# Performance work log

Hardware: AMD Instinct MI355X
Metric: run time of the kernel (lower is better)

## Reference

```python
import jax, jax.numpy as jnp
import numpy as np

B, HGT, WID, D, NS = 4, 64, 128, 128, 2
LN_EPS = 1e-5

def layer_norm(x, g, b):
    m = jnp.mean(x, axis=-1, keepdims=True)
    v = jnp.mean((x - m) ** 2, axis=-1, keepdims=True)
    return (x - m) * jax.lax.rsqrt(v + LN_EPS) * g + b

def setup_inputs() -> dict:
    key = jax.random.key(0)
    ks = jax.random.split(key, 8)
    src = jax.random.normal(ks[0], (B, HGT * WID, D), jnp.float32)
    L = (HGT // NS) * (WID // NS)  # 2048
    s = 0.05
    return {
        "source": src,
        "target": src,  # identical -> self-attention branch in original
        "shifted_window_attn_mask": jax.random.normal(ks[1], (NS * NS, L, L), jnp.float32),
        "shifted_window_attn_mask_1d": jnp.zeros((NS, WID // NS, WID // NS), jnp.float32),
        "height": HGT,
        "width": WID,
        "attn_num_splits": NS,
        "with_shift": 1,
        "Wq": jax.random.normal(ks[2], (D, D), jnp.float32) * s,
        "Wk": jax.random.normal(ks[3], (D, D), jnp.float32) * s,
        "Wv": jax.random.normal(ks[4], (D, D), jnp.float32) * s,
        "Wm": jax.random.normal(ks[5], (D, D), jnp.float32) * s,
        "g1": jnp.ones((D,), jnp.float32),
        "b1": jnp.zeros((D,), jnp.float32),
        "W1": jax.random.normal(ks[6], (2 * D, 8 * D), jnp.float32) * s,
        "W2": jax.random.normal(ks[7], (8 * D, D), jnp.float32) * s,
        "g2": jnp.ones((D,), jnp.float32),
        "b2": jnp.zeros((D,), jnp.float32),
    }

def _shifted_window_self_attn(q, k, v, ns, with_shift, h, w, attn_mask):
    b, _, c = q.shape
    hh, ww = h // ns, w // ns  # window sizes
    sh, sw = hh // 2, ww // 2
    L = hh * ww

    def to_windows(x):
        x = x.reshape(b, h, w, c)
        if with_shift:
            x = jnp.roll(x, shift=(-sh, -sw), axis=(1, 2))
        # (b, ns, hh, ns, ww, c) -> (b*ns*ns, hh*ww, c)
        x = x.reshape(b, ns, hh, ns, ww, c).transpose(0, 1, 3, 2, 4, 5)
        return x.reshape(b * ns * ns, L, c)

    qw, kw, vw = to_windows(q), to_windows(k), to_windows(v)
    scores = jnp.einsum("bqc,bkc->bqk", qw, kw) / (c ** 0.5)  # (b*ns^2, L, L)
    if with_shift:
        scores = (scores.reshape(b, ns * ns, L, L) + attn_mask).reshape(b * ns * ns, L, L)
    attn = jax.nn.softmax(scores, axis=-1)
    out = jnp.einsum("bqk,bkc->bqc", attn, vw)
    # merge windows back
    out = out.reshape(b, ns, ns, hh, ww, c).transpose(0, 1, 3, 2, 4, 5).reshape(b, h, w, c)
    if with_shift:
        out = jnp.roll(out, shift=(sh, sw), axis=(1, 2))
    return out.reshape(b, h * w, c)

def reference(source, target, shifted_window_attn_mask, shifted_window_attn_mask_1d,
              height, width, attn_num_splits, with_shift,
              Wq, Wk, Wv, Wm, g1, b1, W1, W2, g2, b2):
    # target == source -> self-attention, attn_num_splits > 1 -> shifted-window path
    q = source @ Wq
    k = target @ Wk
    v = target @ Wv
    message = _shifted_window_self_attn(q, k, v, attn_num_splits, with_shift,
                                        height, width, shifted_window_attn_mask)
    message = layer_norm(message @ Wm, g1, b1)
    h = jnp.concatenate([source, message], axis=-1)  # (B, HW, 2D)
    message = jax.nn.gelu(h @ W1, approximate=False) @ W2
    message = layer_norm(message, g2, b2)
    return source + message
```

## Files before the change

kernel.cpp:

```cpp
#include <hip/hip_runtime.h>

typedef unsigned short u16;
typedef __bf16 bf16x8 __attribute__((ext_vector_type(8)));
typedef float f32x4 __attribute__((ext_vector_type(4)));

#define MFMA(a, b, c) __builtin_amdgcn_mfma_f32_16x16x32_bf16(a, b, c, 0, 0, 0)


__device__ __forceinline__ u16 f2b(float f) {
  unsigned u = __builtin_bit_cast(unsigned, f);
  u += 0x7fffu + ((u >> 16) & 1u);
  return (u16)(u >> 16);
}
__device__ __forceinline__ float b2f(u16 h) {
  unsigned u = (unsigned)h << 16;
  return __builtin_bit_cast(float, u);
}
__device__ __forceinline__ void glds16(const u16* g, u16* l) {
  __builtin_amdgcn_global_load_lds((const __attribute__((address_space(1))) void*)g,
                                   (__attribute__((address_space(3))) void*)l, 16, 0, 0);
}

#define QW_OFF   ((size_t)0)
#define KW_OFF   ((size_t)8 << 20)
#define VBUF_OFF ((size_t)16 << 20)
#define O1_OFF   ((size_t)24 << 20)
#define O2_OFF   ((size_t)40 << 20)
#define HID_OFF  ((size_t)0)
#define SRCB_OFF ((size_t)64 << 20)
#define MSG1_OFF ((size_t)72 << 20)
#define L1_OFF   ((size_t)80 << 20)
#define L2P_OFF  (((size_t)80 << 20) + 131072)
#define WQT_OFF  (((size_t)80 << 20) + 262144)
#define WKT_OFF  (WQT_OFF + 32768)
#define WVT_OFF  (WQT_OFF + 65536)
#define WMT_OFF  (WQT_OFF + 98304)
#define W1T_OFF  (WQT_OFF + 131072)
#define W2T_OFF  (WQT_OFF + 655360)

__global__ void k_prep(const float* __restrict__ wq, const float* __restrict__ wk,
                       const float* __restrict__ wv, const float* __restrict__ wm,
                       const float* __restrict__ w1, const float* __restrict__ w2,
                       u16* __restrict__ wqt, u16* __restrict__ wkt,
                       u16* __restrict__ wvt, u16* __restrict__ wmt,
                       u16* __restrict__ w1t, u16* __restrict__ w2t) {
  int t = blockIdx.x * 256 + threadIdx.x;
  if (t < 65536) {
    int m = t >> 14, loc = t & 16383;
    int n = loc >> 7, k = loc & 127;
    const float* s = (m == 0) ? wq : (m == 1) ? wk : (m == 2) ? wv : wm;
    u16* d = (m == 0) ? wqt : (m == 1) ? wkt : (m == 2) ? wvt : wmt;
    const float sc = (m == 0) ? 0.08838834764831845f : 1.0f;
    d[n * 128 + k] = f2b(s[k * 128 + n] * sc);
  } else if (t < 65536 + 262144) {
    int loc = t - 65536;
    int n = loc >> 8, k = loc & 255;
    w1t[n * 256 + k] = f2b(w1[k * 1024 + n]);
  } else if (t < 65536 + 262144 + 131072) {
    int loc = t - 327680;
    int n = loc >> 10, k = loc & 1023;
    w2t[n * 1024 + k] = f2b(w2[k * 128 + n]);
  }
}

__global__ __launch_bounds__(256, 2)
void k_qkv(const float* __restrict__ src,
           const u16* __restrict__ wtq, const u16* __restrict__ wtk,
           const u16* __restrict__ wtv,
           u16* __restrict__ qw, u16* __restrict__ kw, u16* __restrict__ vbuf,
           u16* __restrict__ srcb) {
  __shared__ __align__(16) u16 At[64 * 136];
  __shared__ __align__(16) u16 Bt[128 * 136];
  const int tid = threadIdx.x, bid = blockIdx.x;
  const int lane = tid & 63, wid = tid >> 6;
  const int l15 = lane & 15, quad = lane >> 4;

  {
    const int row = tid >> 2, part = tid & 3;
    const int t = bid * 64 + row;
    const int g = t >> 11, p = t & 2047;
    const int b = g >> 2, wi = (g >> 1) & 1, wj = g & 1;
    const int ii = p >> 6, jj = p & 63;
    const int y = (wi * 32 + ii + 16) & 63;
    const int x = (wj * 64 + jj + 32) & 127;
    const int srow = b * 8192 + y * 128 + x;
    const float4* sp = (const float4*)(src + srow * 128) + part * 8;
    u16* lp = &At[row * 136 + part * 32];
    u16* gp = srcb + srow * 128 + part * 32;
#pragma unroll
    for (int q = 0; q < 8; ++q) {
      float4 v = sp[q];
      ushort4 h = make_ushort4(f2b(v.x), f2b(v.y), f2b(v.z), f2b(v.w));
      *(ushort4*)(lp + q * 4) = h;
      *(ushort4*)(gp + q * 4) = h;
    }
  }
  __syncthreads();

  bf16x8 afrag[4];
  const int arow = wid * 16 + l15;
#pragma unroll
  for (int kk = 0; kk < 4; ++kk)
    afrag[kk] = *(const bf16x8*)&At[arow * 136 + kk * 32 + quad * 8];

  const f32x4 fz = {0.f, 0.f, 0.f, 0.f};
#pragma unroll 1
  for (int m = 0; m < 3; ++m) {
    const u16* wp = (m == 0) ? wtq : (m == 1) ? wtk : wtv;
    {
      const int n = tid >> 1, half = tid & 1;
      const uint4* sp = (const uint4*)(wp + n * 128 + half * 64);
      uint4* dp = (uint4*)&Bt[n * 136 + half * 64];
#pragma unroll
      for (int q = 0; q < 8; ++q) dp[q] = sp[q];
    }
    __syncthreads();
    f32x4 acc[8];
#pragma unroll
    for (int nt = 0; nt < 8; ++nt) acc[nt] = fz;
#pragma unroll
    for (int kk = 0; kk < 4; ++kk) {
#pragma unroll
      for (int nt = 0; nt < 8; ++nt) {
        bf16x8 bfr = *(const bf16x8*)&Bt[(nt * 16 + l15) * 136 + kk * 32 + quad * 8];
        acc[nt] = MFMA(afrag[kk], bfr, acc[nt]);
      }
    }
    const int t0 = bid * 64 + wid * 16 + quad * 4;
    if (m < 2) {
      u16* dst = (m == 0) ? qw : kw;
#pragma unroll
      for (int nt = 0; nt < 8; ++nt) {
        const int d = nt * 16 + l15;
#pragma unroll
        for (int r = 0; r < 4; ++r) dst[(t0 + r) * 128 + d] = f2b(acc[nt][r]);
      }
    } else {
      const int g = bid >> 5;
      const int p0 = t0 & 2047;
#pragma unroll
      for (int nt = 0; nt < 8; ++nt) {
        const int d = nt * 16 + l15;
        ushort4 hv = make_ushort4(f2b(acc[nt][0]), f2b(acc[nt][1]),
                                  f2b(acc[nt][2]), f2b(acc[nt][3]));
        *(ushort4*)&vbuf[g * 262144 + d * 2048 + p0] = hv;
      }
    }
    __syncthreads();
  }
}

__global__ __launch_bounds__(256, 2)
void k_attn(const u16* __restrict__ qw, const u16* __restrict__ kw,
            const u16* __restrict__ vbuf, const float* __restrict__ mask,
            u16* __restrict__ o1, u16* __restrict__ o2,
            float* __restrict__ l1, float* __restrict__ l2) {
  __shared__ __align__(16) u16 Kt[2][64 * 128];
  __shared__ __align__(16) u16 Vt[2][128 * 64];
  __shared__ __align__(16) u16 Pt[128 * 40];
  const int tid = threadIdx.x;
  const int bid = (blockIdx.x & 7) * 64 + (blockIdx.x >> 3);
  const int lane = tid & 63, wid = tid >> 6;
  const int l15 = lane & 15, quad = lane >> 4;
  const int b = bid & 3, w = (bid >> 2) & 3, half = (bid >> 4) & 1, qb = bid >> 5;
  const int g = b * 4 + w;
  const int k0 = half * 1024;
  const u16* kbase = kw + g * 262144 + k0 * 128;
  const u16* vbase = vbuf + g * 262144 + k0;
  const int qrow0 = qb * 128 + wid * 32;
  const float* mlane = mask + (size_t)w * 4194304 + (size_t)(qrow0 + quad * 4) * 2048 + k0 + l15;

  int offk[4], offv[4], dstb[4];
#pragma unroll
  for (int j = 0; j < 4; ++j) {
    const int s = wid * 256 + j * 64 + lane;
    const int rk = s >> 4, bk = (s & 15) ^ (rk & 15);
    offk[j] = rk * 128 + bk * 8;
    const int dv = s >> 3, bv = (s & 7) ^ (dv & 7);
    offv[j] = dv * 2048 + bv * 8;
    dstb[j] = (wid * 256 + j * 64) * 8;
  }

  bf16x8 qfrag[2][4];
#pragma unroll
  for (int qs = 0; qs < 2; ++qs) {
    const u16* qp = qw + g * 262144 + (qrow0 + qs * 16 + l15) * 128 + quad * 8;
#pragma unroll
    for (int kk = 0; kk < 4; ++kk) qfrag[qs][kk] = *(const bf16x8*)(qp + kk * 32);
  }
  const f32x4 fz = {0.f, 0.f, 0.f, 0.f};
  f32x4 o[2][8];
#pragma unroll
  for (int qs = 0; qs < 2; ++qs)
#pragma unroll
    for (int nt = 0; nt < 8; ++nt) o[qs][nt] = fz;
  float lr[2][4] = {{0.f, 0.f, 0.f, 0.f}, {0.f, 0.f, 0.f, 0.f}};
  const float L2E = 1.4426950408889634f;

#pragma unroll
  for (int j = 0; j < 4; ++j) {
    glds16(kbase + offk[j], &Kt[0][dstb[j]]);
    glds16(vbase + offv[j], &Vt[0][dstb[j]]);
  }
  float mpf[16];
#pragma unroll
  for (int qs = 0; qs < 2; ++qs)
#pragma unroll
    for (int ntl = 0; ntl < 2; ++ntl)
#pragma unroll
      for (int r = 0; r < 4; ++r)
        mpf[qs * 8 + ntl * 4 + r] = mlane[(qs * 16 + r) * 2048 + ntl * 16];

#pragma unroll 1
  for (int kt = 0; kt < 16; ++kt) {
    const int p = kt & 1;
    __syncthreads();
    if (kt < 15) {
      const u16* kb = kbase + (kt + 1) * 8192;
      const u16* vb = vbase + (kt + 1) * 64;
#pragma unroll
      for (int j = 0; j < 4; ++j) {
        glds16(kb + offk[j], &Kt[p ^ 1][dstb[j]]);
        glds16(vb + offv[j], &Vt[p ^ 1][dstb[j]]);
      }
    }
#pragma unroll
    for (int ks = 0; ks < 2; ++ks) {
      float mn[16];
      const bool hasn = (kt < 15) || (ks == 0);
      const int ncol = kt * 64 + 32 + ks * 32;
      if (hasn) {
#pragma unroll
        for (int qs = 0; qs < 2; ++qs)
#pragma unroll
          for (int ntl = 0; ntl < 2; ++ntl)
#pragma unroll
            for (int r = 0; r < 4; ++r)
              mn[qs * 8 + ntl * 4 + r] = mlane[(qs * 16 + r) * 2048 + ncol + ntl * 16];
      }
      f32x4 s[2][2];
#pragma unroll
      for (int qs = 0; qs < 2; ++qs)
#pragma unroll
        for (int ntl = 0; ntl < 2; ++ntl)
#pragma unroll
          for (int r = 0; r < 4; ++r) s[qs][ntl][r] = mpf[qs * 8 + ntl * 4 + r];
#pragma unroll
      for (int kk = 0; kk < 4; ++kk)
#pragma unroll
        for (int ntl = 0; ntl < 2; ++ntl) {
          bf16x8 kfr = *(const bf16x8*)&Kt[p][(ks * 32 + ntl * 16 + l15) * 128 +
                                             (((kk * 4 + quad) ^ l15) * 8)];
          s[0][ntl] = MFMA(qfrag[0][kk], kfr, s[0][ntl]);
          s[1][ntl] = MFMA(qfrag[1][kk], kfr, s[1][ntl]);
        }
#pragma unroll
      for (int qs = 0; qs < 2; ++qs)
#pragma unroll
        for (int ntl = 0; ntl < 2; ++ntl)
#pragma unroll
          for (int r = 0; r < 4; ++r) {
            const float pv = exp2f(s[qs][ntl][r] * L2E);
            lr[qs][r] += pv;
            Pt[(wid * 32 + qs * 16 + quad * 4 + r) * 40 + ntl * 16 + l15] = f2b(pv);
          }
      bf16x8 pf0 = *(const bf16x8*)&Pt[(wid * 32 + l15) * 40 + quad * 8];
      bf16x8 pf1 = *(const bf16x8*)&Pt[(wid * 32 + 16 + l15) * 40 + quad * 8];
#pragma unroll
      for (int nt = 0; nt < 8; ++nt) {
        bf16x8 vfr = *(const bf16x8*)&Vt[p][(nt * 16 + l15) * 64 +
                                            (((ks * 4 + quad) ^ (l15 & 7)) * 8)];
        o[0][nt] = MFMA(pf0, vfr, o[0][nt]);
        o[1][nt] = MFMA(pf1, vfr, o[1][nt]);
      }
      if (hasn) {
#pragma unroll
        for (int i = 0; i < 16; ++i) mpf[i] = mn[i];
      }
    }
  }

#pragma unroll
  for (int off = 1; off < 16; off <<= 1)
#pragma unroll
    for (int qs = 0; qs < 2; ++qs)
#pragma unroll
      for (int r = 0; r < 4; ++r) lr[qs][r] += __shfl_xor(lr[qs][r], off, 16);
  u16* op = half ? o2 : o1;
  float* lp = half ? l2 : l1;
#pragma unroll
  for (int qs = 0; qs < 2; ++qs) {
    const int t0 = g * 2048 + qrow0 + qs * 16 + quad * 4;
#pragma unroll
    for (int r = 0; r < 4; ++r) {
      const float inv = 1.f / lr[qs][r];
#pragma unroll
      for (int nt = 0; nt < 8; ++nt)
        op[(size_t)(t0 + r) * 128 + nt * 16 + l15] = f2b(o[qs][nt][r] * inv);
      if (l15 == 0) lp[t0 + r] = lr[qs][r];
    }
  }
}

__global__ __launch_bounds__(256, 2)
void k_wmln(const u16* __restrict__ o1, const u16* __restrict__ o2,
            const float* __restrict__ l1, const float* __restrict__ l2,
            const u16* __restrict__ wmt, const float* __restrict__ g1,
            const float* __restrict__ b1, u16* __restrict__ msg1) {
  __shared__ __align__(16) u16 At[64 * 136];
  __shared__ __align__(16) u16 Bt[128 * 136];
  const int tid = threadIdx.x, bid = blockIdx.x;
  const int lane = tid & 63, wid = tid >> 6;
  const int l15 = lane & 15, quad = lane >> 4;
  {
    const int row = tid >> 2, part = tid & 3;
    const int m = bid * 64 + row;
    const float la = l1[m], lb = l2[m];
    const float wA = la / (la + lb), wB = lb / (la + lb);
    const u16* p1 = o1 + (size_t)m * 128 + part * 32;
    const u16* p2 = o2 + (size_t)m * 128 + part * 32;
    u16* lp = &At[row * 136 + part * 32];
#pragma unroll
    for (int q = 0; q < 4; ++q) {
      ushort4 xa = *(const ushort4*)(p1 + q * 8);
      ushort4 xb = *(const ushort4*)(p1 + q * 8 + 4);
      ushort4 ya = *(const ushort4*)(p2 + q * 8);
      ushort4 yb = *(const ushort4*)(p2 + q * 8 + 4);
      ushort4 ha = make_ushort4(f2b(b2f(xa.x) * wA + b2f(ya.x) * wB),
                                f2b(b2f(xa.y) * wA + b2f(ya.y) * wB),
                                f2b(b2f(xa.z) * wA + b2f(ya.z) * wB),
                                f2b(b2f(xa.w) * wA + b2f(ya.w) * wB));
      ushort4 hb = make_ushort4(f2b(b2f(xb.x) * wA + b2f(yb.x) * wB),
                                f2b(b2f(xb.y) * wA + b2f(yb.y) * wB),
                                f2b(b2f(xb.z) * wA + b2f(yb.z) * wB),
                                f2b(b2f(xb.w) * wA + b2f(yb.w) * wB));
      *(ushort4*)(lp + q * 8) = ha;
      *(ushort4*)(lp + q * 8 + 4) = hb;
    }
  }
  {
    const int n = tid >> 1, half = tid & 1;
    const uint4* sp = (const uint4*)(wmt + n * 128 + half * 64);
    uint4* dp = (uint4*)&Bt[n * 136 + half * 64];
#pragma unroll
    for (int q = 0; q < 8; ++q) dp[q] = sp[q];
  }
  __syncthreads();
  bf16x8 afrag[4];
  const int arow = wid * 16 + l15;
#pragma unroll
  for (int kk = 0; kk < 4; ++kk)
    afrag[kk] = *(const bf16x8*)&At[arow * 136 + kk * 32 + quad * 8];
  const f32x4 fz = {0.f, 0.f, 0.f, 0.f};
  f32x4 acc[8];
#pragma unroll
  for (int nt = 0; nt < 8; ++nt) acc[nt] = fz;
#pragma unroll
  for (int kk = 0; kk < 4; ++kk)
#pragma unroll
    for (int nt = 0; nt < 8; ++nt) {
      bf16x8 bfr = *(const bf16x8*)&Bt[(nt * 16 + l15) * 136 + kk * 32 + quad * 8];
      acc[nt] = MFMA(afrag[kk], bfr, acc[nt]);
    }
  float sum[4] = {0, 0, 0, 0}, sq[4] = {0, 0, 0, 0};
#pragma unroll
  for (int nt = 0; nt < 8; ++nt)
#pragma unroll
    for (int r = 0; r < 4; ++r) {
      const float v = acc[nt][r];
      sum[r] += v;
      sq[r] += v * v;
    }
#pragma unroll
  for (int off = 1; off < 16; off <<= 1)
#pragma unroll
    for (int r = 0; r < 4; ++r) {
      sum[r] += __shfl_xor(sum[r], off, 16);
      sq[r] += __shfl_xor(sq[r], off, 16);
    }
  float mean[4], rstd[4];
#pragma unroll
  for (int r = 0; r < 4; ++r) {
    mean[r] = sum[r] * (1.f / 128.f);
    const float var = sq[r] * (1.f / 128.f) - mean[r] * mean[r];
    rstd[r] = rsqrtf(var + 1e-5f);
  }
  const int t0 = bid * 64 + wid * 16 + quad * 4;
#pragma unroll
  for (int nt = 0; nt < 8; ++nt) {
    const int d = nt * 16 + l15;
    const float gg = g1[d], bb = b1[d];
#pragma unroll
    for (int r = 0; r < 4; ++r) {
      const int tt = t0 + r;
      const int gw = tt >> 11, pp = tt & 2047;
      const int bb2 = gw >> 2, wi = (gw >> 1) & 1, wj = gw & 1;
      const int ii = pp >> 6, jj = pp & 63;
      const int yy = (wi * 32 + ii + 16) & 63;
      const int xx = (wj * 64 + jj + 32) & 127;
      msg1[(bb2 * 8192 + yy * 128 + xx) * 128 + d] =
          f2b((acc[nt][r] - mean[r]) * rstd[r] * gg + bb);
    }
  }
}

__global__ __launch_bounds__(256, 3)
void k_mlp1(const u16* __restrict__ srcb, const u16* __restrict__ msg1,
            const u16* __restrict__ w1t, u16* __restrict__ hid) {
  __shared__ __align__(16) u16 At[64 * 72];
  __shared__ __align__(16) u16 Bt[256 * 72];
  const int tid = threadIdx.x, bid = blockIdx.x;
  const int rb = bid >> 2, nb = bid & 3;
  const int lane = tid & 63, wid = tid >> 6;
  const int l15 = lane & 15, quad = lane >> 4;
  const f32x4 fz = {0.f, 0.f, 0.f, 0.f};
  f32x4 acc[16];
#pragma unroll
  for (int nt = 0; nt < 16; ++nt) acc[nt] = fz;
#pragma unroll 1
  for (int kc = 0; kc < 4; ++kc) {
    __syncthreads();
    {
      const int row = tid >> 2, part = tid & 3;
      const u16* sp0 = (kc < 2) ? srcb : msg1;
      const uint4* sp = (const uint4*)(sp0 + (rb * 64 + row) * 128 + (kc & 1) * 64 + part * 16);
      uint4* dp = (uint4*)&At[row * 72 + part * 16];
      dp[0] = sp[0];
      dp[1] = sp[1];
    }
    {
      const uint4* sp = (const uint4*)(w1t + (nb * 256 + tid) * 256 + kc * 64);
      uint4* dp = (uint4*)&Bt[tid * 72];
#pragma unroll
      for (int q = 0; q < 8; ++q) dp[q] = sp[q];
    }
    __syncthreads();
#pragma unroll
    for (int kk = 0; kk < 2; ++kk) {
      bf16x8 a = *(const bf16x8*)&At[(wid * 16 + l15) * 72 + kk * 32 + quad * 8];
#pragma unroll
      for (int nt = 0; nt < 16; ++nt) {
        bf16x8 b = *(const bf16x8*)&Bt[(nt * 16 + l15) * 72 + kk * 32 + quad * 8];
        acc[nt] = MFMA(a, b, acc[nt]);
      }
    }
  }
  const int t0 = rb * 64 + wid * 16 + quad * 4;
#pragma unroll
  for (int nt = 0; nt < 16; ++nt) {
    const int n = nb * 256 + nt * 16 + l15;
#pragma unroll
    for (int r = 0; r < 4; ++r) {
      const float x = acc[nt][r];
      const float y = 0.5f * x * (1.f + erff(x * 0.70710678118654752f));
      hid[(size_t)(t0 + r) * 1024 + n] = f2b(y);
    }
  }
}

__global__ __launch_bounds__(256, 2)
void k_mlp2(const u16* __restrict__ hid, const u16* __restrict__ w2t,
            const float* __restrict__ g2, const float* __restrict__ b2,
            const float* __restrict__ src, float* __restrict__ out) {
  __shared__ __align__(16) u16 At[64 * 72];
  __shared__ __align__(16) u16 Bt[128 * 72];
  const int tid = threadIdx.x, bid = blockIdx.x;
  const int lane = tid & 63, wid = tid >> 6;
  const int l15 = lane & 15, quad = lane >> 4;
  const f32x4 fz = {0.f, 0.f, 0.f, 0.f};
  f32x4 acc[8];
#pragma unroll
  for (int nt = 0; nt < 8; ++nt) acc[nt] = fz;
#pragma unroll 1
  for (int kc = 0; kc < 16; ++kc) {
    __syncthreads();
    {
      const int row = tid >> 2, part = tid & 3;
      const uint4* sp = (const uint4*)(hid + (size_t)(bid * 64 + row) * 1024 + kc * 64 + part * 16);
      uint4* dp = (uint4*)&At[row * 72 + part * 16];
      dp[0] = sp[0];
      dp[1] = sp[1];
    }
    {
      const int n = tid >> 1, half = tid & 1;
      const uint4* sp = (const uint4*)(w2t + n * 1024 + kc * 64 + half * 32);
      uint4* dp = (uint4*)&Bt[n * 72 + half * 32];
#pragma unroll
      for (int q = 0; q < 4; ++q) dp[q] = sp[q];
    }
    __syncthreads();
#pragma unroll
    for (int kk = 0; kk < 2; ++kk) {
      bf16x8 a = *(const bf16x8*)&At[(wid * 16 + l15) * 72 + kk * 32 + quad * 8];
#pragma unroll
      for (int nt = 0; nt < 8; ++nt) {
        bf16x8 b = *(const bf16x8*)&Bt[(nt * 16 + l15) * 72 + kk * 32 + quad * 8];
        acc[nt] = MFMA(a, b, acc[nt]);
      }
    }
  }
  float sum[4] = {0, 0, 0, 0}, sq[4] = {0, 0, 0, 0};
#pragma unroll
  for (int nt = 0; nt < 8; ++nt)
#pragma unroll
    for (int r = 0; r < 4; ++r) {
      const float v = acc[nt][r];
      sum[r] += v;
      sq[r] += v * v;
    }
#pragma unroll
  for (int off = 1; off < 16; off <<= 1)
#pragma unroll
    for (int r = 0; r < 4; ++r) {
      sum[r] += __shfl_xor(sum[r], off, 16);
      sq[r] += __shfl_xor(sq[r], off, 16);
    }
  float mean[4], rstd[4];
#pragma unroll
  for (int r = 0; r < 4; ++r) {
    mean[r] = sum[r] * (1.f / 128.f);
    const float var = sq[r] * (1.f / 128.f) - mean[r] * mean[r];
    rstd[r] = rsqrtf(var + 1e-5f);
  }
  const int t0 = bid * 64 + wid * 16 + quad * 4;
#pragma unroll
  for (int nt = 0; nt < 8; ++nt) {
    const int d = nt * 16 + l15;
    const float gg = g2[d], bb = b2[d];
#pragma unroll
    for (int r = 0; r < 4; ++r) {
      const int idx = (t0 + r) * 128 + d;
      out[idx] = src[idx] + (acc[nt][r] - mean[r]) * rstd[r] * gg + bb;
    }
  }
}

extern "C" void kernel_launch(void* const* d_in, const int* in_sizes, int n_in,
                              void* d_out, int out_size, void* d_ws, size_t ws_size,
                              hipStream_t stream) {
  const float* src  = (const float*)d_in[0];
  const float* mask = (const float*)d_in[2];
  const float* Wq = (const float*)d_in[8];
  const float* Wk = (const float*)d_in[9];
  const float* Wv = (const float*)d_in[10];
  const float* Wm = (const float*)d_in[11];
  const float* g1 = (const float*)d_in[12];
  const float* b1 = (const float*)d_in[13];
  const float* W1 = (const float*)d_in[14];
  const float* W2 = (const float*)d_in[15];
  const float* g2 = (const float*)d_in[16];
  const float* b2 = (const float*)d_in[17];
  char* ws = (char*)d_ws;
  u16* qw   = (u16*)(ws + QW_OFF);
  u16* kw   = (u16*)(ws + KW_OFF);
  u16* vbuf = (u16*)(ws + VBUF_OFF);
  u16* o1   = (u16*)(ws + O1_OFF);
  u16* o2   = (u16*)(ws + O2_OFF);
  float* l1 = (float*)(ws + L1_OFF);
  float* l2 = (float*)(ws + L2P_OFF);
  u16* hid  = (u16*)(ws + HID_OFF);
  u16* srcb = (u16*)(ws + SRCB_OFF);
  u16* msg1 = (u16*)(ws + MSG1_OFF);
  u16* wqt = (u16*)(ws + WQT_OFF);
  u16* wkt = (u16*)(ws + WKT_OFF);
  u16* wvt = (u16*)(ws + WVT_OFF);
  u16* wmt = (u16*)(ws + WMT_OFF);
  u16* w1t = (u16*)(ws + W1T_OFF);
  u16* w2t = (u16*)(ws + W2T_OFF);

  k_prep<<<1792, 256, 0, stream>>>(Wq, Wk, Wv, Wm, W1, W2, wqt, wkt, wvt, wmt, w1t, w2t);
  k_qkv<<<512, 256, 0, stream>>>(src, wqt, wkt, wvt, qw, kw, vbuf, srcb);
  k_attn<<<512, 256, 0, stream>>>(qw, kw, vbuf, mask, o1, o2, l1, l2);
  k_wmln<<<512, 256, 0, stream>>>(o1, o2, l1, l2, wmt, g1, b1, msg1);
  k_mlp1<<<2048, 256, 0, stream>>>(srcb, msg1, w1t, hid);
  k_mlp2<<<512, 256, 0, stream>>>(hid, w2t, g2, b2, src, (float*)d_out);
}
```

Baseline: 323.0 us.

## Fuse MLP kernels keeping hidden in LDS; load V fragments directly in attention

The two MLP kernels become one. Each block computes a 64-wide chunk of the GELU hidden activations into LDS and feeds it straight into the second GEMM, so the large bf16 hidden tensor is never written to or read back from global memory. Weight tiles are staged with async global-to-LDS loads using a swizzled layout. In attention, V is now read from global directly into registers instead of being double-buffered in LDS, and the block-to-tile mapping is reordered so consecutive blocks share a window. Risks: the fused MLP has a single-buffered weight pipeline with syncs every chunk and only 512 blocks, and the direct V loads add global-load latency inside the inner loop.

```diff
diff --git a/kernel.cpp b/kernel.cpp
--- a/kernel.cpp
+++ b/kernel.cpp
@@ -26,7 +26,6 @@
 #define VBUF_OFF ((size_t)16 << 20)
 #define O1_OFF   ((size_t)24 << 20)
 #define O2_OFF   ((size_t)40 << 20)
-#define HID_OFF  ((size_t)0)
 #define SRCB_OFF ((size_t)64 << 20)
 #define MSG1_OFF ((size_t)72 << 20)
 #define L1_OFF   ((size_t)80 << 20)
@@ -156,28 +155,25 @@
             u16* __restrict__ o1, u16* __restrict__ o2,
             float* __restrict__ l1, float* __restrict__ l2) {
   __shared__ __align__(16) u16 Kt[2][64 * 128];
-  __shared__ __align__(16) u16 Vt[2][128 * 64];
   __shared__ __align__(16) u16 Pt[128 * 40];
   const int tid = threadIdx.x;
   const int bid = (blockIdx.x & 7) * 64 + (blockIdx.x >> 3);
   const int lane = tid & 63, wid = tid >> 6;
   const int l15 = lane & 15, quad = lane >> 4;
-  const int b = bid & 3, w = (bid >> 2) & 3, half = (bid >> 4) & 1, qb = bid >> 5;
-  const int g = b * 4 + w;
+  const int qb = bid & 15, half = (bid >> 4) & 1, g = bid >> 5;
+  const int w = g & 3;
   const int k0 = half * 1024;
   const u16* kbase = kw + g * 262144 + k0 * 128;
   const u16* vbase = vbuf + g * 262144 + k0;
   const int qrow0 = qb * 128 + wid * 32;
   const float* mlane = mask + (size_t)w * 4194304 + (size_t)(qrow0 + quad * 4) * 2048 + k0 + l15;
 
-  int offk[4], offv[4], dstb[4];
+  int offk[4], dstb[4];
 #pragma unroll
   for (int j = 0; j < 4; ++j) {
     const int s = wid * 256 + j * 64 + lane;
     const int rk = s >> 4, bk = (s & 15) ^ (rk & 15);
     offk[j] = rk * 128 + bk * 8;
-    const int dv = s >> 3, bv = (s & 7) ^ (dv & 7);
-    offv[j] = dv * 2048 + bv * 8;
     dstb[j] = (wid * 256 + j * 64) * 8;
   }
 
@@ -198,10 +194,7 @@
   const float L2E = 1.4426950408889634f;
 
 #pragma unroll
-  for (int j = 0; j < 4; ++j) {
-    glds16(kbase + offk[j], &Kt[0][dstb[j]]);
-    glds16(vbase + offv[j], &Vt[0][dstb[j]]);
-  }
+  for (int j = 0; j < 4; ++j) glds16(kbase + offk[j], &Kt[0][dstb[j]]);
   float mpf[16];
 #pragma unroll
   for (int qs = 0; qs < 2; ++qs)
@@ -217,15 +210,16 @@
     __syncthreads();
     if (kt < 15) {
       const u16* kb = kbase + (kt + 1) * 8192;
-      const u16* vb = vbase + (kt + 1) * 64;
-#pragma unroll
-      for (int j = 0; j < 4; ++j) {
-        glds16(kb + offk[j], &Kt[p ^ 1][dstb[j]]);
-        glds16(vb + offv[j], &Vt[p ^ 1][dstb[j]]);
-      }
+#pragma unroll
+      for (int j = 0; j < 4; ++j) glds16(kb + offk[j], &Kt[p ^ 1][dstb[j]]);
     }
 #pragma unroll
     for (int ks = 0; ks < 2; ++ks) {
+      bf16x8 vf[8];
+      const u16* vp = vbase + kt * 64 + ks * 32 + quad * 8;
+#pragma unroll
+      for (int nt = 0; nt < 8; ++nt)
+        vf[nt] = *(const bf16x8*)(vp + (size_t)(nt * 16 + l15) * 2048);
       float mn[16];
       const bool hasn = (kt < 15) || (ks == 0);
       const int ncol = kt * 64 + 32 + ks * 32;
@@ -268,10 +262,8 @@
       bf16x8 pf1 = *(const bf16x8*)&Pt[(wid * 32 + 16 + l15) * 40 + quad * 8];
 #pragma unroll
       for (int nt = 0; nt < 8; ++nt) {
-        bf16x8 vfr = *(const bf16x8*)&Vt[p][(nt * 16 + l15) * 64 +
-                                            (((ks * 4 + quad) ^ (l15 & 7)) * 8)];
-        o[0][nt] = MFMA(pf0, vfr, o[0][nt]);
-        o[1][nt] = MFMA(pf1, vfr, o[1][nt]);
+        o[0][nt] = MFMA(pf0, vf[nt], o[0][nt]);
+        o[1][nt] = MFMA(pf1, vf[nt], o[1][nt]);
       }
       if (hasn) {
 #pragma unroll
@@ -404,107 +396,96 @@
   }
 }
 
-__global__ __launch_bounds__(256, 3)
-void k_mlp1(const u16* __restrict__ srcb, const u16* __restrict__ msg1,
-            const u16* __restrict__ w1t, u16* __restrict__ hid) {
-  __shared__ __align__(16) u16 At[64 * 72];
-  __shared__ __align__(16) u16 Bt[256 * 72];
-  const int tid = threadIdx.x, bid = blockIdx.x;
-  const int rb = bid >> 2, nb = bid & 3;
-  const int lane = tid & 63, wid = tid >> 6;
-  const int l15 = lane & 15, quad = lane >> 4;
-  const f32x4 fz = {0.f, 0.f, 0.f, 0.f};
-  f32x4 acc[16];
-#pragma unroll
-  for (int nt = 0; nt < 16; ++nt) acc[nt] = fz;
-#pragma unroll 1
-  for (int kc = 0; kc < 4; ++kc) {
-    __syncthreads();
-    {
-      const int row = tid >> 2, part = tid & 3;
-      const u16* sp0 = (kc < 2) ? srcb : msg1;
-      const uint4* sp = (const uint4*)(sp0 + (rb * 64 + row) * 128 + (kc & 1) * 64 + part * 16);
-      uint4* dp = (uint4*)&At[row * 72 + part * 16];
-      dp[0] = sp[0];
-      dp[1] = sp[1];
-    }
-    {
-      const uint4* sp = (const uint4*)(w1t + (nb * 256 + tid) * 256 + kc * 64);
-      uint4* dp = (uint4*)&Bt[tid * 72];
-#pragma unroll
-      for (int q = 0; q < 8; ++q) dp[q] = sp[q];
-    }
-    __syncthreads();
-#pragma unroll
-    for (int kk = 0; kk < 2; ++kk) {
-      bf16x8 a = *(const bf16x8*)&At[(wid * 16 + l15) * 72 + kk * 32 + quad * 8];
-#pragma unroll
-      for (int nt = 0; nt < 16; ++nt) {
-        bf16x8 b = *(const bf16x8*)&Bt[(nt * 16 + l15) * 72 + kk * 32 + quad * 8];
-        acc[nt] = MFMA(a, b, acc[nt]);
-      }
-    }
-  }
-  const int t0 = rb * 64 + wid * 16 + quad * 4;
-#pragma unroll
-  for (int nt = 0; nt < 16; ++nt) {
-    const int n = nb * 256 + nt * 16 + l15;
-#pragma unroll
-    for (int r = 0; r < 4; ++r) {
-      const float x = acc[nt][r];
-      const float y = 0.5f * x * (1.f + erff(x * 0.70710678118654752f));
-      hid[(size_t)(t0 + r) * 1024 + n] = f2b(y);
-    }
-  }
-}
-
 __global__ __launch_bounds__(256, 2)
-void k_mlp2(const u16* __restrict__ hid, const u16* __restrict__ w2t,
-            const float* __restrict__ g2, const float* __restrict__ b2,
-            const float* __restrict__ src, float* __restrict__ out) {
-  __shared__ __align__(16) u16 At[64 * 72];
-  __shared__ __align__(16) u16 Bt[128 * 72];
+void k_mlp(const u16* __restrict__ srcb, const u16* __restrict__ msg1,
+           const u16* __restrict__ w1t, const u16* __restrict__ w2t,
+           const float* __restrict__ g2, const float* __restrict__ b2,
+           const float* __restrict__ src, float* __restrict__ out) {
+  __shared__ __align__(16) u16 Bt1[64 * 256];
+  __shared__ __align__(16) u16 Bt2[128 * 64];
+  __shared__ __align__(16) u16 Ht[64 * 72];
   const int tid = threadIdx.x, bid = blockIdx.x;
   const int lane = tid & 63, wid = tid >> 6;
   const int l15 = lane & 15, quad = lane >> 4;
+
+  int off1[8], db1[8], off2[4], db2[4];
+#pragma unroll
+  for (int j = 0; j < 8; ++j) {
+    const int s = wid * 512 + j * 64 + lane;
+    const int r = s >> 5, c = s & 31;
+    off1[j] = r * 256 + (c ^ (r & 15)) * 8;
+    db1[j] = (wid * 512 + j * 64) * 8;
+  }
+#pragma unroll
+  for (int j = 0; j < 4; ++j) {
+    const int s = wid * 256 + j * 64 + lane;
+    const int r = s >> 3, c = s & 7;
+    off2[j] = r * 1024 + (c ^ (r & 7)) * 8;
+    db2[j] = (wid * 256 + j * 64) * 8;
+  }
+
+  bf16x8 afrag[8];
+  {
+    const int row = bid * 64 + wid * 16 + l15;
+    const u16* sp = srcb + (size_t)row * 128 + quad * 8;
+    const u16* mp = msg1 + (size_t)row * 128 + quad * 8;
+#pragma unroll
+    for (int kk = 0; kk < 4; ++kk) {
+      afrag[kk] = *(const bf16x8*)(sp + kk * 32);
+      afrag[kk + 4] = *(const bf16x8*)(mp + kk * 32);
+    }
+  }
   const f32x4 fz = {0.f, 0.f, 0.f, 0.f};
-  f32x4 acc[8];
-#pragma unroll
-  for (int nt = 0; nt < 8; ++nt) acc[nt] = fz;
+  f32x4 oacc[8];
+#pragma unroll
+  for (int nt = 0; nt < 8; ++nt) oacc[nt] = fz;
+
 #pragma unroll 1
-  for (int kc = 0; kc < 16; ++kc) {
+  for (int hc = 0; hc < 16; ++hc) {
     __syncthreads();
-    {
-      const int row = tid >> 2, part = tid & 3;
-      const uint4* sp = (const uint4*)(hid + (size_t)(bid * 64 + row) * 1024 + kc * 64 + part * 16);
-      uint4* dp = (uint4*)&At[row * 72 + part * 16];
-      dp[0] = sp[0];
-      dp[1] = sp[1];
-    }
-    {
-      const int n = tid >> 1, half = tid & 1;
-      const uint4* sp = (const uint4*)(w2t + n * 1024 + kc * 64 + half * 32);
-      uint4* dp = (uint4*)&Bt[n * 72 + half * 32];
-#pragma unroll
-      for (int q = 0; q < 4; ++q) dp[q] = sp[q];
-    }
+#pragma unroll
+    for (int j = 0; j < 8; ++j) glds16(w1t + hc * 16384 + off1[j], &Bt1[db1[j]]);
+#pragma unroll
+    for (int j = 0; j < 4; ++j) glds16(w2t + hc * 64 + off2[j], &Bt2[db2[j]]);
     __syncthreads();
-#pragma unroll
-    for (int kk = 0; kk < 2; ++kk) {
-      bf16x8 a = *(const bf16x8*)&At[(wid * 16 + l15) * 72 + kk * 32 + quad * 8];
+
+    f32x4 hacc[4];
+#pragma unroll
+    for (int nt = 0; nt < 4; ++nt) hacc[nt] = fz;
+#pragma unroll
+    for (int kk = 0; kk < 8; ++kk)
+#pragma unroll
+      for (int nt = 0; nt < 4; ++nt) {
+        bf16x8 b1 = *(const bf16x8*)&Bt1[(nt * 16 + l15) * 256 +
+                                         (((kk * 4 + quad) ^ l15) * 8)];
+        hacc[nt] = MFMA(afrag[kk], b1, hacc[nt]);
+      }
+#pragma unroll
+    for (int nt = 0; nt < 4; ++nt)
+#pragma unroll
+      for (int r = 0; r < 4; ++r) {
+        const float x = hacc[nt][r];
+        const float y = 0.5f * x * (1.f + erff(x * 0.70710678118654752f));
+        Ht[(wid * 16 + quad * 4 + r) * 72 + nt * 16 + l15] = f2b(y);
+      }
+    bf16x8 hf0 = *(const bf16x8*)&Ht[(wid * 16 + l15) * 72 + quad * 8];
+    bf16x8 hf1 = *(const bf16x8*)&Ht[(wid * 16 + l15) * 72 + 32 + quad * 8];
+#pragma unroll
+    for (int kk2 = 0; kk2 < 2; ++kk2)
 #pragma unroll
       for (int nt = 0; nt < 8; ++nt) {
-        bf16x8 b = *(const bf16x8*)&Bt[(nt * 16 + l15) * 72 + kk * 32 + quad * 8];
-        acc[nt] = MFMA(a, b, acc[nt]);
-      }
-    }
-  }
+        bf16x8 b2f_ = *(const bf16x8*)&Bt2[(nt * 16 + l15) * 64 +
+                                           (((kk2 * 4 + quad) ^ (l15 & 7)) * 8)];
+        oacc[nt] = MFMA(kk2 ? hf1 : hf0, b2f_, oacc[nt]);
+      }
+  }
+
   float sum[4] = {0, 0, 0, 0}, sq[4] = {0, 0, 0, 0};
 #pragma unroll
   for (int nt = 0; nt < 8; ++nt)
 #pragma unroll
     for (int r = 0; r < 4; ++r) {
-      const float v = acc[nt][r];
+      const float v = oacc[nt][r];
       sum[r] += v;
       sq[r] += v * v;
     }
@@ -530,7 +511,7 @@
 #pragma unroll
     for (int r = 0; r < 4; ++r) {
       const int idx = (t0 + r) * 128 + d;
-      out[idx] = src[idx] + (acc[nt][r] - mean[r]) * rstd[r] * gg + bb;
+      out[idx] = src[idx] + (oacc[nt][r] - mean[r]) * rstd[r] * gg + bb;
     }
   }
 }
@@ -558,7 +539,6 @@
   u16* o2   = (u16*)(ws + O2_OFF);
   float* l1 = (float*)(ws + L1_OFF);
   float* l2 = (float*)(ws + L2P_OFF);
-  u16* hid  = (u16*)(ws + HID_OFF);
   u16* srcb = (u16*)(ws + SRCB_OFF);
   u16* msg1 = (u16*)(ws + MSG1_OFF);
   u16* wqt = (u16*)(ws + WQT_OFF);
@@ -572,6 +552,5 @@
   k_qkv<<<512, 256, 0, stream>>>(src, wqt, wkt, wvt, qw, kw, vbuf, srcb);
   k_attn<<<512, 256, 0, stream>>>(qw, kw, vbuf, mask, o1, o2, l1, l2);
   k_wmln<<<512, 256, 0, stream>>>(o1, o2, l1, l2, wmt, g1, b1, msg1);
-  k_mlp1<<<2048, 256, 0, stream>>>(srcb, msg1, w1t, hid);
-  k_mlp2<<<512, 256, 0, stream>>>(hid, w2t, g2, b2, src, (float*)d_out);
-}
+  k_mlp<<<512, 256, 0, stream>>>(srcb, msg1, w1t, w2t, g2, b2, src, (float*)d_out);
+}
```

Result: faster. 316.6 us (-2.0%).
